# Optimization experiments

Measured on AMD Instinct MI355X. Metric: run time of the kernel, lower is better.

Reference implementation:

```python
import jax, jax.numpy as jnp
import numpy as np

K = 64          # tagset size (len(tag_to_ix))
START = 62      # start_tag_id
STOP = 63       # stop_tag_id
NEG = -10000.0


def setup_inputs() -> dict:
    key = jax.random.key(0)
    k1, k2, k3 = jax.random.split(key, 3)
    B, T = 1024, 512
    feats = jax.random.normal(k1, (B, T, K), dtype=jnp.float32)
    tags = jax.random.randint(k2, (B, T), 0, K, dtype=jnp.int32)
    # learned transition matrix; transitions[i, j] = score of moving from tag j to tag i
    transitions = jax.random.normal(k3, (K, K), dtype=jnp.float32)
    transitions = transitions.at[START, :].set(NEG).at[:, STOP].set(NEG)
    return {"feats": feats, "tags": tags, "transitions": transitions}


def reference(feats, tags, transitions):
    B, T, _ = feats.shape
    # log_alpha init: -10000 everywhere except start tag (matches torch code; feats[:,0] unused)
    alpha0 = jnp.full((B, K), NEG, dtype=feats.dtype).at[:, START].set(0.0)

    def step(alpha, feat_t):
        # alpha: [B, K]; new_alpha[b, i] = lse_j(transitions[i, j] + alpha[b, j]) + feat_t[b, i]
        new_alpha = jax.nn.logsumexp(transitions[None, :, :] + alpha[:, None, :], axis=-1) + feat_t
        return new_alpha, None

    feats_seq = jnp.transpose(feats[:, 1:, :], (1, 0, 2))  # [T-1, B, K]
    alpha, _ = jax.lax.scan(step, alpha0, feats_seq)
    forward_score = jax.nn.logsumexp(alpha, axis=-1)  # [B]

    # gold path score: sum_t transitions[tags[t], tags[t-1]] + feats[t, tags[t]], t = 1..T-1
    trans_score = transitions[tags[:, 1:], tags[:, :-1]].sum(axis=1)  # [B]
    emit_score = jnp.take_along_axis(feats[:, 1:, :], tags[:, 1:, None], axis=2)[..., 0].sum(axis=1)  # [B]
    gold_score = trans_score + emit_score

    return jnp.mean(forward_score - gold_score)
```

## Files before the change

kernel.cpp:

```cpp
#include <hip/hip_runtime.h>


#define BB 1024
#define TT 512
#define KK 64
#define START_TAG 62

#define RLF(v, l) __uint_as_float((unsigned)__builtin_amdgcn_readlane((int)__float_as_uint(v), (l)))

__global__ __launch_bounds__(64, 1) void crf_forward_kernel(
    const float* __restrict__ feats,
    const int*   __restrict__ tags,
    const float* __restrict__ trans,
    float*       __restrict__ diff)
{
  const int lane = threadIdx.x;
  const int b    = blockIdx.x;

  float4 e4[16];
  {
    const float4* trow = (const float4*)(trans + lane * KK);
    #pragma unroll
    for (int jc = 0; jc < 16; ++jc) {
      float4 tv = trow[jc];
      e4[jc] = make_float4(__expf(tv.x), __expf(tv.y),
                           __expf(tv.z), __expf(tv.w));
    }
  }

  const float* fb = feats + (size_t)b * TT * KK + lane;

  float upf[7];
  #pragma unroll
  for (int d = 0; d < 7; ++d) upf[d] = fb[(size_t)(1 + d) * KK];

  float beta  = (lane == START_TAG) ? 1.0f : 0.0f;
  int   esum  = 0;
  float f_cur = __expf(upf[0]);

  for (int g = 0; g < 73; ++g) {
    #pragma unroll
    for (int d = 0; d < 7; ++d) {
      const int t = 1 + g * 7 + d;

      float4 a0 = {0.f, 0.f, 0.f, 0.f};
      float4 a1 = {0.f, 0.f, 0.f, 0.f};
      #pragma unroll
      for (int jc = 0; jc < 16; jc += 2) {
        a0.x = fmaf(e4[jc].x,     RLF(beta, 4*jc + 0), a0.x);
        a0.y = fmaf(e4[jc].y,     RLF(beta, 4*jc + 1), a0.y);
        a0.z = fmaf(e4[jc].z,     RLF(beta, 4*jc + 2), a0.z);
        a0.w = fmaf(e4[jc].w,     RLF(beta, 4*jc + 3), a0.w);
        a1.x = fmaf(e4[jc + 1].x, RLF(beta, 4*jc + 4), a1.x);
        a1.y = fmaf(e4[jc + 1].y, RLF(beta, 4*jc + 5), a1.y);
        a1.z = fmaf(e4[jc + 1].z, RLF(beta, 4*jc + 6), a1.z);
        a1.w = fmaf(e4[jc + 1].w, RLF(beta, 4*jc + 7), a1.w);
      }
      float z = ((a0.x + a1.x) + (a0.y + a1.y)) +
                ((a0.z + a1.z) + (a0.w + a1.w));

      int tn = t + 7; if (tn > TT - 1) tn = TT - 1;
      upf[d] = fb[(size_t)tn * KK];

      unsigned zb = (unsigned)__builtin_amdgcn_readlane((int)__float_as_uint(z), 0);
      float s = __uint_as_float(0x7F000000u - (zb & 0x7F800000u));
      esum += (int)((zb >> 23) & 0xFFu) - 127;
      beta = (z * f_cur) * s;

      f_cur = __expf((d < 6) ? upf[d + 1] : upf[0]);
    }
  }

  float bs = beta;
  #pragma unroll
  for (int off = 32; off; off >>= 1) bs += __shfl_xor(bs, off);
  float fwd = __logf(bs) + (float)esum * 0.6931471805599453f;

  const int* tg = tags + b * TT;
  float gs = 0.0f;
  for (int tt = 1 + lane; tt < TT; tt += 64) {
    int tc = tg[tt];
    int tp = tg[tt - 1];
    gs += trans[tc * KK + tp]
        + feats[(size_t)b * TT * KK + (size_t)tt * KK + tc];
  }
  #pragma unroll
  for (int off = 32; off; off >>= 1) gs += __shfl_xor(gs, off);

  if (lane == 0) diff[b] = fwd - gs;
}

__global__ __launch_bounds__(1024) void reduce_mean_kernel(
    const float* __restrict__ diff, float* __restrict__ out)
{
  __shared__ float part[16];
  const int tid = threadIdx.x;
  float v = diff[tid];
  #pragma unroll
  for (int off = 32; off; off >>= 1) v += __shfl_xor(v, off);
  if ((tid & 63) == 0) part[tid >> 6] = v;
  __syncthreads();
  if (tid < 16) {
    float s = part[tid];
    #pragma unroll
    for (int off = 8; off; off >>= 1) s += __shfl_xor(s, off);
    if (tid == 0) out[0] = s * (1.0f / 1024.0f);
  }
}

extern "C" void kernel_launch(void* const* d_in, const int* in_sizes, int n_in,
                              void* d_out, int out_size, void* d_ws, size_t ws_size,
                              hipStream_t stream) {
  const float* feats = (const float*)d_in[0];
  const int*   tags  = (const int*)d_in[1];
  const float* trans = (const float*)d_in[2];
  float* out  = (float*)d_out;
  float* diff = (float*)d_ws;

  crf_forward_kernel<<<dim3(BB), dim3(64), 0, stream>>>(feats, tags, trans, diff);
  reduce_mean_kernel<<<dim3(1), dim3(1024), 0, stream>>>(diff, out);
}
```

Before: 283.6 us.

## Hand-write CRF forward recurrence in inline GCN assembly with explicit readlane scheduling

Replaces the compiler-generated forward recurrence with an inline-assembly loop. It pins the exponentiated transition row in fixed VGPRs, batches eight readlanes ahead of their FMAs, and software-pipelines the feature prefetch through a six-register rotating buffer with manual waitcnt. The first step is peeled by seeding the recurrence with the START-tag column, and the exponent bias correction is folded into the epilogue. The aim is to cut per-step latency on the serial chain. In exchange the code relies on hard-coded registers and iteration counts that are fragile and hard to verify.

```diff
diff --git a/kernel.cpp b/kernel.cpp
--- a/kernel.cpp
+++ b/kernel.cpp
@@ -6,7 +6,59 @@
 #define KK 64
 #define START_TAG 62
 
-#define RLF(v, l) __uint_as_float((unsigned)__builtin_amdgcn_readlane((int)__float_as_uint(v), (l)))
+#define RL(S, L)     "v_readlane_b32 s" #S ", v26, " #L "\n\t"
+#define FM(A, S, E)  "v_fmac_f32 v" #A ", s" #S ", v" #E "\n\t"
+#define ML(A, S, E)  "v_mul_f32 v" #A ", s" #S ", v" #E "\n\t"
+#define EM(R)        "v_mul_f32 v" #R ", s61, v" #R "\n\t"
+#define EX(R)        "v_exp_f32 v" #R ", v" #R "\n\t"
+#define EM8(a,b,c,d,e,f,g,h) EM(a) EM(b) EM(c) EM(d) EM(e) EM(f) EM(g) EM(h)
+#define EX8(a,b,c,d,e,f,g,h) EX(a) EX(b) EX(c) EX(d) EX(e) EX(f) EX(g) EX(h)
+
+#define MATVEC \
+  RL(40,0)  RL(41,1)  RL(42,2)  RL(43,3)  RL(44,4)  RL(45,5)  RL(46,6)  RL(47,7)  \
+  ML(10,40,32) ML(11,41,33) ML(12,42,34) ML(13,43,35) ML(14,44,36) ML(15,45,37) ML(16,46,38) ML(17,47,39) \
+  RL(48,8)  RL(49,9)  RL(50,10) RL(51,11) RL(52,12) RL(53,13) RL(54,14) RL(55,15) \
+  FM(10,48,40) FM(11,49,41) FM(12,50,42) FM(13,51,43) FM(14,52,44) FM(15,53,45) FM(16,54,46) FM(17,55,47) \
+  RL(40,16) RL(41,17) RL(42,18) RL(43,19) RL(44,20) RL(45,21) RL(46,22) RL(47,23) \
+  FM(10,40,48) FM(11,41,49) FM(12,42,50) FM(13,43,51) FM(14,44,52) FM(15,45,53) FM(16,46,54) FM(17,47,55) \
+  RL(48,24) RL(49,25) RL(50,26) RL(51,27) RL(52,28) RL(53,29) RL(54,30) RL(55,31) \
+  FM(10,48,56) FM(11,49,57) FM(12,50,58) FM(13,51,59) FM(14,52,60) FM(15,53,61) FM(16,54,62) FM(17,55,63) \
+  RL(40,32) RL(41,33) RL(42,34) RL(43,35) RL(44,36) RL(45,37) RL(46,38) RL(47,39) \
+  FM(10,40,64) FM(11,41,65) FM(12,42,66) FM(13,43,67) FM(14,44,68) FM(15,45,69) FM(16,46,70) FM(17,47,71) \
+  RL(48,40) RL(49,41) RL(50,42) RL(51,43) RL(52,44) RL(53,45) RL(54,46) RL(55,47) \
+  FM(10,48,72) FM(11,49,73) FM(12,50,74) FM(13,51,75) FM(14,52,76) FM(15,53,77) FM(16,54,78) FM(17,55,79) \
+  RL(40,48) RL(41,49) RL(42,50) RL(43,51) RL(44,52) RL(45,53) RL(46,54) RL(47,55) \
+  FM(10,40,80) FM(11,41,81) FM(12,42,82) FM(13,43,83) FM(14,44,84) FM(15,45,85) FM(16,46,86) FM(17,47,87) \
+  RL(48,56) RL(49,57) RL(50,58) RL(51,59) RL(52,60) RL(53,61) RL(54,62) RL(55,63) \
+  FM(10,48,88) \
+  "v_readlane_b32 s56, v10, 0\n\t" \
+  FM(11,49,89) FM(12,50,90) FM(13,51,91) FM(14,52,92) FM(15,53,93) FM(16,54,94) FM(17,55,95)
+
+#define BODY(LDS, NXT, FC, FN) \
+  "v_min_u32 v29, %[vmax], v27\n\t" \
+  "global_load_dword " LDS ", v29, %[fb]\n\t" \
+  "v_add_u32 v27, 0x100, v27\n\t" \
+  "s_waitcnt vmcnt(5)\n\t" \
+  "v_mul_f32 " FN ", s61, " NXT "\n\t" \
+  "v_exp_f32 " FN ", " FN "\n\t" \
+  MATVEC \
+  "s_lshr_b32 s57, s56, 23\n\t" \
+  "s_and_b32 s57, s57, 0xff\n\t" \
+  "s_add_i32 s58, s58, s57\n\t" \
+  "s_and_b32 s59, s56, 0x7f800000\n\t" \
+  "s_sub_u32 s59, 0x7f000000, s59\n\t" \
+  "v_add_f32 v10, v10, v11\n\t" \
+  "v_add_f32 v12, v12, v13\n\t" \
+  "v_add_f32 v14, v14, v15\n\t" \
+  "v_add_f32 v16, v16, v17\n\t" \
+  "v_mul_f32 v28, s59, " FC "\n\t" \
+  "v_add_f32 v10, v10, v12\n\t" \
+  "v_add_f32 v14, v14, v16\n\t" \
+  "v_add_f32 v10, v10, v14\n\t" \
+  "v_mul_f32 v26, v10, v28\n\t"
+
+#define LDE(A, B, OFF) \
+  "global_load_dwordx4 v[" #A ":" #B "], %[ta], off offset:" #OFF "\n\t"
 
 __global__ __launch_bounds__(64, 1) void crf_forward_kernel(
     const float* __restrict__ feats,
@@ -17,64 +69,85 @@
   const int lane = threadIdx.x;
   const int b    = blockIdx.x;
 
-  float4 e4[16];
-  {
-    const float4* trow = (const float4*)(trans + lane * KK);
-    #pragma unroll
-    for (int jc = 0; jc < 16; ++jc) {
-      float4 tv = trow[jc];
-      e4[jc] = make_float4(__expf(tv.x), __expf(tv.y),
-                           __expf(tv.z), __expf(tv.w));
-    }
-  }
+  unsigned long long fb64 = (unsigned long long)(uintptr_t)feats;
+  unsigned long long ta64 = (unsigned long long)(uintptr_t)(trans + lane * KK);
+  unsigned voff = ((unsigned)b * (TT * KK) + (unsigned)lane) * 4u;
+  unsigned vmax = voff + 511u * 256u;
 
-  const float* fb = feats + (size_t)b * TT * KK + lane;
+  float p_out;
+  int   esum_raw;
 
-  float upf[7];
-  #pragma unroll
-  for (int d = 0; d < 7; ++d) upf[d] = fb[(size_t)(1 + d) * KK];
+  asm volatile(
+    "s_mov_b32 s58, 0\n\t"
+    "s_mov_b32 s61, 0x3fb8aa3b\n\t"
+    "s_movk_i32 s60, 85\n\t"
+    LDE(32,35,0)   LDE(36,39,16)  LDE(40,43,32)  LDE(44,47,48)
+    LDE(48,51,64)  LDE(52,55,80)  LDE(56,59,96)  LDE(60,63,112)
+    LDE(64,67,128) LDE(68,71,144) LDE(72,75,160) LDE(76,79,176)
+    LDE(80,83,192) LDE(84,87,208) LDE(88,91,224) LDE(92,95,240)
+    "v_add_u32 v27, 0x100, %[voff]\n\t"
+    "global_load_dword v28, v27, %[fb]\n\t"
+    "v_add_u32 v27, 0x100, v27\n\t"
+    "global_load_dword v18, v27, %[fb]\n\t"
+    "v_add_u32 v27, 0x100, v27\n\t"
+    "global_load_dword v19, v27, %[fb]\n\t"
+    "v_add_u32 v27, 0x100, v27\n\t"
+    "global_load_dword v20, v27, %[fb]\n\t"
+    "v_add_u32 v27, 0x100, v27\n\t"
+    "global_load_dword v21, v27, %[fb]\n\t"
+    "v_add_u32 v27, 0x100, v27\n\t"
+    "global_load_dword v22, v27, %[fb]\n\t"
+    "v_add_u32 v27, 0x100, v27\n\t"
+    "global_load_dword v23, v27, %[fb]\n\t"
+    "v_add_u32 v27, 0x100, v27\n\t"
+    "s_waitcnt vmcnt(0)\n\t"
+    EM8(32,33,34,35,36,37,38,39) EM8(40,41,42,43,44,45,46,47)
+    EM8(48,49,50,51,52,53,54,55) EM8(56,57,58,59,60,61,62,63)
+    EM8(64,65,66,67,68,69,70,71) EM8(72,73,74,75,76,77,78,79)
+    EM8(80,81,82,83,84,85,86,87) EM8(88,89,90,91,92,93,94,95)
+    EX8(32,33,34,35,36,37,38,39) EX8(40,41,42,43,44,45,46,47)
+    EX8(48,49,50,51,52,53,54,55) EX8(56,57,58,59,60,61,62,63)
+    EX8(64,65,66,67,68,69,70,71) EX8(72,73,74,75,76,77,78,79)
+    EX8(80,81,82,83,84,85,86,87) EX8(88,89,90,91,92,93,94,95)
+    "v_mul_f32 v28, s61, v28\n\t"
+    "v_exp_f32 v28, v28\n\t"
+    "v_mul_f32 v26, v28, v94\n\t"
+    "v_mul_f32 v24, s61, v18\n\t"
+    "v_exp_f32 v24, v24\n\t"
+    "1:\n\t"
+    BODY("v18", "v19", "v24", "v25")
+    BODY("v19", "v20", "v25", "v24")
+    BODY("v20", "v21", "v24", "v25")
+    BODY("v21", "v22", "v25", "v24")
+    BODY("v22", "v23", "v24", "v25")
+    BODY("v23", "v18", "v25", "v24")
+    "s_sub_u32 s60, s60, 1\n\t"
+    "s_cmp_lg_u32 s60, 0\n\t"
+    "s_cbranch_scc1 1b\n\t"
+    "v_mov_b32 %[pO], v26\n\t"
+    "s_mov_b32 %[eO], s58\n\t"
+    : [pO] "=&v"(p_out), [eO] "=&s"(esum_raw)
+    : [fb] "s"(fb64), [ta] "v"(ta64), [voff] "v"(voff), [vmax] "v"(vmax)
+    : "memory",
+      "v10","v11","v12","v13","v14","v15","v16","v17","v18","v19",
+      "v20","v21","v22","v23","v24","v25","v26","v27","v28","v29",
+      "v32","v33","v34","v35","v36","v37","v38","v39",
+      "v40","v41","v42","v43","v44","v45","v46","v47",
+      "v48","v49","v50","v51","v52","v53","v54","v55",
+      "v56","v57","v58","v59","v60","v61","v62","v63",
+      "v64","v65","v66","v67","v68","v69","v70","v71",
+      "v72","v73","v74","v75","v76","v77","v78","v79",
+      "v80","v81","v82","v83","v84","v85","v86","v87",
+      "v88","v89","v90","v91","v92","v93","v94","v95",
+      "s40","s41","s42","s43","s44","s45","s46","s47",
+      "s48","s49","s50","s51","s52","s53","s54","s55",
+      "s56","s57","s58","s59","s60","s61");
 
-  float beta  = (lane == START_TAG) ? 1.0f : 0.0f;
-  int   esum  = 0;
-  float f_cur = __expf(upf[0]);
-
-  for (int g = 0; g < 73; ++g) {
-    #pragma unroll
-    for (int d = 0; d < 7; ++d) {
-      const int t = 1 + g * 7 + d;
-
-      float4 a0 = {0.f, 0.f, 0.f, 0.f};
-      float4 a1 = {0.f, 0.f, 0.f, 0.f};
-      #pragma unroll
-      for (int jc = 0; jc < 16; jc += 2) {
-        a0.x = fmaf(e4[jc].x,     RLF(beta, 4*jc + 0), a0.x);
-        a0.y = fmaf(e4[jc].y,     RLF(beta, 4*jc + 1), a0.y);
-        a0.z = fmaf(e4[jc].z,     RLF(beta, 4*jc + 2), a0.z);
-        a0.w = fmaf(e4[jc].w,     RLF(beta, 4*jc + 3), a0.w);
-        a1.x = fmaf(e4[jc + 1].x, RLF(beta, 4*jc + 4), a1.x);
-        a1.y = fmaf(e4[jc + 1].y, RLF(beta, 4*jc + 5), a1.y);
-        a1.z = fmaf(e4[jc + 1].z, RLF(beta, 4*jc + 6), a1.z);
-        a1.w = fmaf(e4[jc + 1].w, RLF(beta, 4*jc + 7), a1.w);
-      }
-      float z = ((a0.x + a1.x) + (a0.y + a1.y)) +
-                ((a0.z + a1.z) + (a0.w + a1.w));
-
-      int tn = t + 7; if (tn > TT - 1) tn = TT - 1;
-      upf[d] = fb[(size_t)tn * KK];
-
-      unsigned zb = (unsigned)__builtin_amdgcn_readlane((int)__float_as_uint(z), 0);
-      float s = __uint_as_float(0x7F000000u - (zb & 0x7F800000u));
-      esum += (int)((zb >> 23) & 0xFFu) - 127;
-      beta = (z * f_cur) * s;
-
-      f_cur = __expf((d < 6) ? upf[d + 1] : upf[0]);
-    }
-  }
-
-  float bs = beta;
+  float bs = p_out;
   #pragma unroll
   for (int off = 32; off; off >>= 1) bs += __shfl_xor(bs, off);
-  float fwd = __logf(bs) + (float)esum * 0.6931471805599453f;
+  float fwd = __logf(bs) +
+              (float)(esum_raw - 127 * 510) * 0.6931471805599453f;
 
   const int* tg = tags + b * TT;
   float gs = 0.0f;
```

Result: slower. 295.4 us (+4.2%).
